# Kernel tuning notes

Hardware: AMD Instinct MI355X
Metric: run time of the kernel (lower is better)

Reference implementation:

```python
import jax, jax.numpy as jnp
import numpy as np

DIM = 12       # model width (l1 out, S5 H)
SEQ = 1600     # SAMPLE_LEN, fixed by BatchNorm1d(SAMPLE_LEN)
P = 8          # STATE_DIM
BATCH = 1024
EPS = 1e-5


def setup_inputs() -> dict:
    key = jax.random.key(0)
    ks = jax.random.split(key, 16)
    rn = lambda k, shape, s=1.0: jax.random.normal(k, shape, jnp.float32) * s
    inp = {}
    inp["x"] = rn(ks[0], (BATCH, SEQ, 1))
    inp["l1_w"] = rn(ks[1], (DIM, 1), 0.5)
    inp["l1_b"] = rn(ks[2], (DIM,), 0.1)
    inp["l2_w"] = rn(ks[3], (1, DIM), 0.3)
    inp["l2_b"] = rn(ks[4], (1,), 0.1)
    inp["bn_gamma"] = jnp.ones((SEQ,), jnp.float32)
    inp["bn_beta"] = jnp.zeros((SEQ,), jnp.float32)
    # S5 parameters for the 3 stacked layers (s5, s5b, s5c), stacked on axis 0.
    # HiPPO-like init: stable (negative real) diagonal, imaginary parts ~ pi*k.
    inp["lam_re"] = -jax.random.uniform(ks[5], (3, P), jnp.float32, 0.1, 1.0)
    inp["lam_im"] = jnp.broadcast_to(np.pi * jnp.arange(P, dtype=jnp.float32), (3, P)) \
                    + 0.1 * rn(ks[6], (3, P))
    inp["b_re"] = rn(ks[7], (3, P, DIM), 1.0 / np.sqrt(DIM))
    inp["b_im"] = rn(ks[8], (3, P, DIM), 1.0 / np.sqrt(DIM))
    inp["c_re"] = rn(ks[9], (3, DIM, P), 1.0 / np.sqrt(P))
    inp["c_im"] = rn(ks[10], (3, DIM, P), 1.0 / np.sqrt(P))
    inp["d"] = rn(ks[11], (3, DIM))
    inp["log_step"] = jnp.log(jax.random.uniform(ks[12], (3, P), jnp.float32, 1e-3, 1e-1))
    return inp


def _s5_layer(u, lam_re, lam_im, b_re, b_im, c_re, c_im, d, log_step):
    """S5 diagonal SSM: ZOH discretization + parallel associative scan.
    u: [B, L, H] real. Returns [B, L, H] real."""
    step = jnp.exp(log_step)                               # [P]
    lam = (lam_re + 1j * lam_im).astype(jnp.complex64)     # [P]
    lam_bar = jnp.exp(lam * step)                          # [P]
    b_bar = ((lam_bar - 1.0) / lam)[:, None] * (b_re + 1j * b_im)  # [P, H]
    # Bu_k = B_bar @ u_k  -> [B, L, P] complex
    bu = (u @ b_bar.real.T) + 1j * (u @ b_bar.imag.T)
    a = jnp.broadcast_to(lam_bar, bu.shape)                # [B, L, P]

    def combine(e1, e2):
        a1, s1 = e1
        a2, s2 = e2
        return a1 * a2, a2 * s1 + s2

    _, xs = jax.lax.associative_scan(combine, (a, bu), axis=1)  # x_k states
    c = c_re + 1j * c_im                                   # [H, P]
    y = 2.0 * jnp.einsum('blp,hp->blh', xs, c).real + u * d
    return y


def reference(x, l1_w, l1_b, l2_w, l2_b, bn_gamma, bn_beta,
              lam_re, lam_im, b_re, b_im, c_re, c_im, d, log_step):
    out = x @ l1_w.T + l1_b                                # [B, L, DIM]
    res = out
    # BatchNorm1d(SEQ) on [B, C=SEQ, L=DIM]: stats over batch and last dim
    mean = out.mean(axis=(0, 2))                           # [SEQ]
    var = out.var(axis=(0, 2))                             # biased, as torch training BN
    out = (out - mean[None, :, None]) * jax.lax.rsqrt(var + EPS)[None, :, None]
    out = out * bn_gamma[None, :, None] + bn_beta[None, :, None]

    out = _s5_layer(out, lam_re[0], lam_im[0], b_re[0], b_im[0], c_re[0], c_im[0], d[0], log_step[0])
    out = jax.nn.relu(out) + res
    res = out
    out = _s5_layer(out, lam_re[1], lam_im[1], b_re[1], b_im[1], c_re[1], c_im[1], d[1], log_step[1])
    out = jax.nn.relu(out) + res
    out = _s5_layer(out, lam_re[2], lam_im[2], b_re[2], b_im[2], c_re[2], c_im[2], d[2], log_step[2])
    return out @ l2_w.T + l2_b                             # [B, L, 1]
```

## Files before the change

kernel.cpp:

```cpp
#include <hip/hip_runtime.h>
#include <cmath>

#define SEQ 1600
#define NB  1024
#define H   12
#define PP  8

typedef float f2 __attribute__((ext_vector_type(2)));

#define O_G0A  0
#define O_G0B  16
#define O_G0C  32
#define O_G1A  48
#define O_G1B  64
#define O_G2A  80
#define O_G2B  96
#define O_LB0R 112
#define O_LB0I 128
#define O_LB1R 144
#define O_LB1I 160
#define O_LB2R 176
#define O_LB2I 192
#define O_C0R  208
#define O_C0I  304
#define O_C1R  400
#define O_C1I  496
#define O_BB1  592
#define O_BB2  784
#define O_FX0  976
#define O_FY0  988
#define O_FZ0  1000
#define O_FW0  1012
#define O_F1X  1024
#define O_F1Y  1036
#define O_F1Z  1048
#define O_CWN  1060
#define O_A6   1076
#define O_A7   1124
#define O_SC   1172
#define PRMF   1174

__device__ __forceinline__ f2 pk_fma_s(f2 a_s, f2 b, f2 c) {
    double d;
    asm("v_pk_fma_f32 %0, %1, %2, %3"
        : "=v"(d)
        : "s"(__builtin_bit_cast(double, a_s)),
          "v"(__builtin_bit_cast(double, b)),
          "v"(__builtin_bit_cast(double, c)));
    return __builtin_bit_cast(f2, d);
}
__device__ __forceinline__ f2 pk_fma_vv(f2 a, f2 b, f2 c) {
    double d;
    asm("v_pk_fma_f32 %0, %1, %2, %3"
        : "=v"(d)
        : "v"(__builtin_bit_cast(double, a)),
          "v"(__builtin_bit_cast(double, b)),
          "v"(__builtin_bit_cast(double, c)));
    return __builtin_bit_cast(f2, d);
}
__device__ __forceinline__ f2 pk_fma_s_blo(f2 a_s, f2 b, f2 c) {
    double d;
    asm("v_pk_fma_f32 %0, %1, %2, %3 op_sel:[0,0,0] op_sel_hi:[1,0,1]"
        : "=v"(d)
        : "s"(__builtin_bit_cast(double, a_s)),
          "v"(__builtin_bit_cast(double, b)),
          "v"(__builtin_bit_cast(double, c)));
    return __builtin_bit_cast(f2, d);
}
__device__ __forceinline__ f2 pk_fma_s_bhi(f2 a_s, f2 b, f2 c) {
    double d;
    asm("v_pk_fma_f32 %0, %1, %2, %3 op_sel:[0,1,0] op_sel_hi:[1,1,1]"
        : "=v"(d)
        : "s"(__builtin_bit_cast(double, a_s)),
          "v"(__builtin_bit_cast(double, b)),
          "v"(__builtin_bit_cast(double, c)));
    return __builtin_bit_cast(f2, d);
}
__device__ __forceinline__ f2 pk_add_s(f2 a_s, f2 b) {
    double d;
    asm("v_pk_add_f32 %0, %1, %2"
        : "=v"(d)
        : "s"(__builtin_bit_cast(double, a_s)),
          "v"(__builtin_bit_cast(double, b)));
    return __builtin_bit_cast(f2, d);
}
__device__ __forceinline__ f2 pk_add_vv(f2 a, f2 b) {
    double d;
    asm("v_pk_add_f32 %0, %1, %2"
        : "=v"(d)
        : "v"(__builtin_bit_cast(double, a)),
          "v"(__builtin_bit_cast(double, b)));
    return __builtin_bit_cast(f2, d);
}
__device__ __forceinline__ f2 cfma_state(f2 s, f2 lbr2_s, f2 lbi2_s, f2 bu) {
    double t, d;
    asm("v_pk_fma_f32 %0, %1, %2, %3 op_sel:[1,0,0] op_sel_hi:[0,1,1] neg_lo:[1,0,0]"
        : "=v"(t)
        : "v"(__builtin_bit_cast(double, s)),
          "s"(__builtin_bit_cast(double, lbi2_s)),
          "v"(__builtin_bit_cast(double, bu)));
    asm("v_pk_fma_f32 %0, %1, %2, %3"
        : "=v"(d)
        : "v"(__builtin_bit_cast(double, s)),
          "s"(__builtin_bit_cast(double, lbr2_s)),
          "v"(t));
    return __builtin_bit_cast(f2, d);
}
__device__ __forceinline__ f2 cmulv(f2 A, f2 B, f2 C) {
    double t, d;
    asm("v_pk_fma_f32 %0, %1, %2, %3 op_sel:[1,1,0] op_sel_hi:[0,1,1] neg_lo:[1,0,0]"
        : "=v"(t)
        : "v"(__builtin_bit_cast(double, B)),
          "v"(__builtin_bit_cast(double, A)),
          "v"(__builtin_bit_cast(double, C)));
    asm("v_pk_fma_f32 %0, %1, %2, %3 op_sel:[0,0,0] op_sel_hi:[1,0,1]"
        : "=v"(d)
        : "v"(__builtin_bit_cast(double, B)),
          "v"(__builtin_bit_cast(double, A)),
          "v"(t));
    return __builtin_bit_cast(f2, d);
}

__global__ __launch_bounds__(256) void k_stats1(const float* __restrict__ x,
                                                float* __restrict__ pS,
                                                float* __restrict__ pQ) {
    int l = blockIdx.x * 256 + threadIdx.x;
    if (l >= SEQ) return;
    int b0 = blockIdx.y * 64;
    float s = 0.f, q = 0.f;
    for (int b = 0; b < 64; ++b) {
        float v = x[(size_t)(b0 + b) * SEQ + l];
        s += v; q += v * v;
    }
    pS[blockIdx.y * SEQ + l] = s;
    pQ[blockIdx.y * SEQ + l] = q;
}

__global__ __launch_bounds__(256)
void k_stats2prep(const float* __restrict__ pS, const float* __restrict__ pQ,
                  const float* __restrict__ w1, const float* __restrict__ b1,
                  const float* __restrict__ gam, const float* __restrict__ bet,
                  float* __restrict__ scale, float* __restrict__ shift,
                  const float* __restrict__ l2w, const float* __restrict__ l2b,
                  const float* __restrict__ lamr, const float* __restrict__ lami,
                  const float* __restrict__ bre, const float* __restrict__ bim,
                  const float* __restrict__ cre, const float* __restrict__ cim,
                  const float* __restrict__ dv,  const float* __restrict__ lstep,
                  float* __restrict__ gprm) {
    const int t = threadIdx.x;
    if (blockIdx.x < 7) {
        int l = blockIdx.x * 256 + t;
        if (l >= SEQ) return;
        float wm = 0, wq = 0, wb = 0, bm = 0, bq = 0;
        for (int h = 0; h < H; h++) {
            float w = w1[h], b = b1[h];
            wm += w; wq += w * w; wb += w * b; bm += b; bq += b * b;
        }
        const float inv = 1.f / 12.f;
        wm *= inv; wq *= inv; wb *= inv; bm *= inv; bq *= inv;
        float s = 0, q = 0;
        for (int k = 0; k < 16; k++) { s += pS[k * SEQ + l]; q += pQ[k * SEQ + l]; }
        float ex = s * (1.f / NB), exx = q * (1.f / NB);
        float mean = ex * wm + bm;
        float e2   = exx * wq + 2.f * ex * wb + bq;
        float var  = e2 - mean * mean;
        float sc   = gam[l] * rsqrtf(var + 1e-5f);
        scale[l] = sc;
        shift[l] = bet[l] - mean * sc;
        return;
    }
    if (t < 48) {
        int h2 = t >> 3, p = t & 7, h = 2 * h2;
        gprm[O_C0R + 2 * t]     = 2.f * cre[h * PP + p];
        gprm[O_C0R + 2 * t + 1] = 2.f * cre[(h + 1) * PP + p];
        gprm[O_C0I + 2 * t]     = -2.f * cim[h * PP + p];
        gprm[O_C0I + 2 * t + 1] = -2.f * cim[(h + 1) * PP + p];
        gprm[O_C1R + 2 * t]     = 2.f * cre[96 + h * PP + p];
        gprm[O_C1R + 2 * t + 1] = 2.f * cre[96 + (h + 1) * PP + p];
        gprm[O_C1I + 2 * t]     = -2.f * cim[96 + h * PP + p];
        gprm[O_C1I + 2 * t + 1] = -2.f * cim[96 + (h + 1) * PP + p];
    }
    if (t < 6) {
        int h = 2 * t;
        gprm[O_FX0 + 2 * t] = w1[h] * dv[h];          gprm[O_FX0 + 2 * t + 1] = w1[h + 1] * dv[h + 1];
        gprm[O_FY0 + 2 * t] = b1[h] * dv[h];          gprm[O_FY0 + 2 * t + 1] = b1[h + 1] * dv[h + 1];
        gprm[O_FZ0 + 2 * t] = dv[h];                  gprm[O_FZ0 + 2 * t + 1] = dv[h + 1];
        gprm[O_FW0 + 2 * t] = w1[h] * dv[H + h];      gprm[O_FW0 + 2 * t + 1] = w1[h + 1] * dv[H + h + 1];
        gprm[O_F1X + 2 * t] = b1[h] * dv[H + h];      gprm[O_F1X + 2 * t + 1] = b1[h + 1] * dv[H + h + 1];
        gprm[O_F1Y + 2 * t] = dv[H + h];              gprm[O_F1Y + 2 * t + 1] = dv[H + h + 1];
        gprm[O_F1Z + 2 * t] = l2w[h] * dv[2 * H + h]; gprm[O_F1Z + 2 * t + 1] = l2w[h + 1] * dv[2 * H + h + 1];
    }
    if (t == 0) {
        float s0 = l2b[0], s1 = 0.f;
        for (int h = 0; h < H; h++) {
            float dw = l2w[h] * dv[2 * H + h];
            s0 += b1[h] * dw; s1 += w1[h] * dw;
        }
        gprm[O_SC + 0] = s0; gprm[O_SC + 1] = s1;
    }
    if (t < 24) {
        int L = t >> 3, p = t & 7;
        float stp = expf(lstep[L * PP + p]);
        float lr = lamr[L * PP + p], li = lami[L * PP + p];
        float er = expf(lr * stp);
        float lbr = er * cosf(li * stp), lbi = er * sinf(li * stp);
        float p2r = lbr * lbr - lbi * lbi, p2i = 2.f * lbr * lbi;
        float p4r = p2r * p2r - p2i * p2i, p4i = 2.f * p2r * p2i;
        float p6r = p4r * p2r - p4i * p2i, p6i = p4r * p2i + p4i * p2r;
        float p7r = p6r * lbr - p6i * lbi, p7i = p6r * lbi + p6i * lbr;
        gprm[O_A6 + 2 * (L * PP + p) + 0] = p6r;
        gprm[O_A6 + 2 * (L * PP + p) + 1] = p6i;
        gprm[O_A7 + 2 * (L * PP + p) + 0] = p7r;
        gprm[O_A7 + 2 * (L * PP + p) + 1] = p7i;
        float den = lr * lr + li * li;
        float fr = ((lbr - 1.f) * lr + lbi * li) / den;
        float fi = (lbi * lr - (lbr - 1.f) * li) / den;
        float sAr = 0, sAi = 0, sBr = 0, sBi = 0, sCr = 0, sCi = 0;
        for (int h = 0; h < H; h++) {
            float brr = bre[L * 96 + p * H + h], bii = bim[L * 96 + p * H + h];
            float vr = fr * brr - fi * bii, vi = fr * bii + fi * brr;
            float w = w1[h], bb = b1[h];
            sAr += w * vr; sAi += w * vi; sBr += bb * vr; sBi += bb * vi; sCr += vr; sCi += vi;
            int fidx = 2 * (h * PP + p);
            if (L == 1)      { gprm[O_BB1 + fidx] = vr; gprm[O_BB1 + fidx + 1] = vi; }
            else if (L == 2) { gprm[O_BB2 + fidx] = vr; gprm[O_BB2 + fidx + 1] = vi; }
        }
        if (L == 0) {
            gprm[O_G0A + 2 * p] = sAr; gprm[O_G0A + 2 * p + 1] = sAi;
            gprm[O_G0B + 2 * p] = sBr; gprm[O_G0B + 2 * p + 1] = sBi;
            gprm[O_G0C + 2 * p] = sCr; gprm[O_G0C + 2 * p + 1] = sCi;
            gprm[O_LB0R + 2 * p] = lbr; gprm[O_LB0R + 2 * p + 1] = lbr;
            gprm[O_LB0I + 2 * p] = lbi; gprm[O_LB0I + 2 * p + 1] = lbi;
        } else if (L == 1) {
            gprm[O_G1A + 2 * p] = sAr; gprm[O_G1A + 2 * p + 1] = sAi;
            gprm[O_G1B + 2 * p] = sBr; gprm[O_G1B + 2 * p + 1] = sBi;
            gprm[O_LB1R + 2 * p] = lbr; gprm[O_LB1R + 2 * p + 1] = lbr;
            gprm[O_LB1I + 2 * p] = lbi; gprm[O_LB1I + 2 * p + 1] = lbi;
        } else {
            gprm[O_G2A + 2 * p] = sAr; gprm[O_G2A + 2 * p + 1] = sAi;
            gprm[O_G2B + 2 * p] = sBr; gprm[O_G2B + 2 * p + 1] = sBi;
            gprm[O_LB2R + 2 * p] = lbr; gprm[O_LB2R + 2 * p + 1] = lbr;
            gprm[O_LB2I + 2 * p] = lbi; gprm[O_LB2I + 2 * p + 1] = lbi;
            float swr = 0, swi = 0;
            for (int hh = 0; hh < H; hh++) {
                float wv = l2w[hh];
                swr += wv * cre[192 + hh * PP + p];
                swi += wv * cim[192 + hh * PP + p];
            }
            gprm[O_CWN + 2 * p + 0] = 2.f * swr; gprm[O_CWN + 2 * p + 1] = -2.f * swi;
        }
    }
}

__device__ __forceinline__ void scan_carry256(f2* S, const float2* a_init,
                                              int lane, int w,
                                              float2 (*aggA)[PP], float2 (*aggS)[PP]) {
    const f2 z2 = {0.f, 0.f};
    f2 A[PP];
#pragma unroll
    for (int p = 0; p < PP; p++) { A[p].x = a_init[p].x; A[p].y = a_init[p].y; }
#pragma unroll
    for (int d = 1; d < 64; d <<= 1) {
#pragma unroll
        for (int p = 0; p < PP; p++) {
            f2 fS, fA;
            fS.x = __shfl_up(S[p].x, (unsigned)d, 64);
            fS.y = __shfl_up(S[p].y, (unsigned)d, 64);
            fA.x = __shfl_up(A[p].x, (unsigned)d, 64);
            fA.y = __shfl_up(A[p].y, (unsigned)d, 64);
            if (lane >= d) {
                S[p] = cmulv(A[p], fS, S[p]);
                A[p] = cmulv(A[p], fA, z2);
            }
        }
    }
    __syncthreads();
    if (lane == 63) {
#pragma unroll
        for (int p = 0; p < PP; p++) {
            aggA[w][p] = make_float2(A[p].x, A[p].y);
            aggS[w][p] = make_float2(S[p].x, S[p].y);
        }
    }
    __syncthreads();
    float eSr[PP], eSi[PP], eAr[PP], eAi[PP];
#pragma unroll
    for (int p = 0; p < PP; p++) {
        float sr = __shfl_up(S[p].x, 1u, 64);
        float si = __shfl_up(S[p].y, 1u, 64);
        float ar = __shfl_up(A[p].x, 1u, 64);
        float ai = __shfl_up(A[p].y, 1u, 64);
        eSr[p] = (lane > 0) ? sr : 0.f;
        eSi[p] = (lane > 0) ? si : 0.f;
        eAr[p] = (lane > 0) ? ar : 1.f;
        eAi[p] = (lane > 0) ? ai : 0.f;
    }
    float Pr[PP], Pi[PP];
#pragma unroll
    for (int p = 0; p < PP; p++) { Pr[p] = 0.f; Pi[p] = 0.f; }
    for (int w2 = 0; w2 < w; w2++) {
#pragma unroll
        for (int p = 0; p < PP; p++) {
            float2 a = aggA[w2][p];
            float2 s = aggS[w2][p];
            float nr = a.x * Pr[p] - a.y * Pi[p] + s.x;
            float ni = a.x * Pi[p] + a.y * Pr[p] + s.y;
            Pr[p] = nr; Pi[p] = ni;
        }
    }
#pragma unroll
    for (int p = 0; p < PP; p++) {
        S[p].x = eAr[p] * Pr[p] - eAi[p] * Pi[p] + eSr[p];
        S[p].y = eAr[p] * Pi[p] + eAi[p] * Pr[p] + eSi[p];
    }
}

__global__ __launch_bounds__(256)
void k_main(const float* __restrict__ x,
            const float* __restrict__ gprm,
            const float* __restrict__ g_scale, const float* __restrict__ g_shift,
            float* __restrict__ out) {
    __shared__ float4 xq[SEQ];
    __shared__ float2 aggA[4][PP], aggS[4][PP];
    const int tid = threadIdx.x, b = blockIdx.x;
    for (int i = tid; i < SEQ; i += 256) {
        float xx = x[(size_t)b * SEQ + i];
        float sc = g_scale[i], sh = g_shift[i];
        xq[i] = make_float4(xx * sc, sc, sh, xx);
    }
    __syncthreads();
    const f2* g0a = (const f2*)(gprm + O_G0A);
    const f2* g0b = (const f2*)(gprm + O_G0B);
    const f2* g0c = (const f2*)(gprm + O_G0C);
    const f2* g1a = (const f2*)(gprm + O_G1A);
    const f2* g1b = (const f2*)(gprm + O_G1B);
    const f2* g2a = (const f2*)(gprm + O_G2A);
    const f2* g2b = (const f2*)(gprm + O_G2B);
    const f2* lb0r = (const f2*)(gprm + O_LB0R);
    const f2* lb0i = (const f2*)(gprm + O_LB0I);
    const f2* lb1r = (const f2*)(gprm + O_LB1R);
    const f2* lb1i = (const f2*)(gprm + O_LB1I);
    const f2* lb2r = (const f2*)(gprm + O_LB2R);
    const f2* lb2i = (const f2*)(gprm + O_LB2I);
    const f2* c0r = (const f2*)(gprm + O_C0R);
    const f2* c0i = (const f2*)(gprm + O_C0I);
    const f2* c1r = (const f2*)(gprm + O_C1R);
    const f2* c1i = (const f2*)(gprm + O_C1I);
    const f2* bb1 = (const f2*)(gprm + O_BB1);
    const f2* bb2 = (const f2*)(gprm + O_BB2);
    const f2* fx0 = (const f2*)(gprm + O_FX0);
    const f2* fy0 = (const f2*)(gprm + O_FY0);
    const f2* fz0 = (const f2*)(gprm + O_FZ0);
    const f2* fw0 = (const f2*)(gprm + O_FW0);
    const f2* f1x = (const f2*)(gprm + O_F1X);
    const f2* f1y = (const f2*)(gprm + O_F1Y);
    const f2* f1z = (const f2*)(gprm + O_F1Z);
    const f2* cwn = (const f2*)(gprm + O_CWN);
    const float Sc0 = gprm[O_SC], Sc1 = gprm[O_SC + 1];
    const int w = tid >> 6, lane = tid & 63;
    const int len = (w == 3) ? 7 : 6;
    const int l0 = (w < 3) ? (w * 384 + lane * 6) : (1152 + lane * 7);
    const float2* aLb = (const float2*)(gprm + ((w == 3) ? O_A7 : O_A6));
    float* orow = out + (size_t)b * SEQ;
    const f2 z2 = {0.f, 0.f};

    f2 s0[PP], car0[PP];

#pragma unroll
    for (int p = 0; p < PP; p++) s0[p] = z2;
#pragma unroll 1
    for (int j = 0; j < len; j++) {
        float4 q = xq[l0 + j];
        float xs = q.x, sc = q.y, sh = q.z;
        f2 xs2 = {xs, xs}, sc2 = {sc, sc}, sh2 = {sh, sh};
#pragma unroll
        for (int p = 0; p < PP; p++) {
            f2 bu = pk_fma_s(g0c[p], sh2, z2);
            bu = pk_fma_s(g0b[p], sc2, bu);
            bu = pk_fma_s(g0a[p], xs2, bu);
            s0[p] = cfma_state(s0[p], lb0r[p], lb0i[p], bu);
        }
    }
    scan_carry256(s0, aLb, lane, w, aggA, aggS);
#pragma unroll
    for (int p = 0; p < PP; p++) car0[p] = s0[p];

    f2 s1[PP];
#pragma unroll
    for (int p = 0; p < PP; p++) s1[p] = z2;
#pragma unroll 1
    for (int j = 0; j < len; j++) {
        float4 q = xq[l0 + j];
        float xs = q.x, sc = q.y, sh = q.z, xx = q.w;
        f2 xs2 = {xs, xs}, sc2 = {sc, sc}, sh2 = {sh, sh}, xx2 = {xx, xx};
#pragma unroll
        for (int p = 0; p < PP; p++) {
            f2 bu = pk_fma_s(g0c[p], sh2, z2);
            bu = pk_fma_s(g0b[p], sc2, bu);
            bu = pk_fma_s(g0a[p], xs2, bu);
            s0[p] = cfma_state(s0[p], lb0r[p], lb0i[p], bu);
        }
        f2 r0p[6], t1[PP];
#pragma unroll
        for (int p = 0; p < PP; p++) t1[p] = z2;
#pragma unroll
        for (int h2 = 0; h2 < 6; h2++) {
            f2 acc = z2;
#pragma unroll
            for (int p = 0; p < PP; p++) {
                acc = pk_fma_s_blo(c0r[h2 * PP + p], s0[p], acc);
                acc = pk_fma_s_bhi(c0i[h2 * PP + p], s0[p], acc);
            }
            acc = pk_fma_s(fx0[h2], xs2, acc);
            acc = pk_fma_s(fy0[h2], sc2, acc);
            acc = pk_fma_s(fz0[h2], sh2, acc);
            acc.x = fmaxf(acc.x, 0.f); acc.y = fmaxf(acc.y, 0.f);
            r0p[h2] = acc;
#pragma unroll
            for (int p = 0; p < PP; p++) {
                t1[p] = pk_fma_s_blo(bb1[(2 * h2) * PP + p], acc, t1[p]);
                t1[p] = pk_fma_s_bhi(bb1[(2 * h2 + 1) * PP + p], acc, t1[p]);
            }
        }
#pragma unroll
        for (int p = 0; p < PP; p++) {
            f2 t = pk_fma_s(g1a[p], xx2, t1[p]);
            t = pk_add_s(g1b[p], t);
            s1[p] = cfma_state(s1[p], lb1r[p], lb1i[p], t);
        }
    }
    scan_carry256(s1, aLb + PP, lane, w, aggA, aggS);

    f2 s2[PP];
#pragma unroll
    for (int p = 0; p < PP; p++) { s0[p] = car0[p]; s2[p] = z2; }
#pragma unroll 1
    for (int j = 0; j < len; j++) {
        int l = l0 + j;
        float4 q = xq[l];
        float xs = q.x, sc = q.y, sh = q.z, xx = q.w;
        f2 xs2 = {xs, xs}, sc2 = {sc, sc}, sh2 = {sh, sh}, xx2 = {xx, xx};
#pragma unroll
        for (int p = 0; p < PP; p++) {
            f2 bu = pk_fma_s(g0c[p], sh2, z2);
            bu = pk_fma_s(g0b[p], sc2, bu);
            bu = pk_fma_s(g0a[p], xs2, bu);
            s0[p] = cfma_state(s0[p], lb0r[p], lb0i[p], bu);
        }
        f2 r0p[6], t1[PP];
#pragma unroll
        for (int p = 0; p < PP; p++) t1[p] = z2;
#pragma unroll
        for (int h2 = 0; h2 < 6; h2++) {
            f2 acc = z2;
#pragma unroll
            for (int p = 0; p < PP; p++) {
                acc = pk_fma_s_blo(c0r[h2 * PP + p], s0[p], acc);
                acc = pk_fma_s_bhi(c0i[h2 * PP + p], s0[p], acc);
            }
            acc = pk_fma_s(fx0[h2], xs2, acc);
            acc = pk_fma_s(fy0[h2], sc2, acc);
            acc = pk_fma_s(fz0[h2], sh2, acc);
            acc.x = fmaxf(acc.x, 0.f); acc.y = fmaxf(acc.y, 0.f);
            r0p[h2] = acc;
#pragma unroll
            for (int p = 0; p < PP; p++) {
                t1[p] = pk_fma_s_blo(bb1[(2 * h2) * PP + p], acc, t1[p]);
                t1[p] = pk_fma_s_bhi(bb1[(2 * h2 + 1) * PP + p], acc, t1[p]);
            }
        }
#pragma unroll
        for (int p = 0; p < PP; p++) {
            f2 t = pk_fma_s(g1a[p], xx2, t1[p]);
            t = pk_add_s(g1b[p], t);
            s1[p] = cfma_state(s1[p], lb1r[p], lb1i[p], t);
        }
        f2 t2[PP], op = z2;
#pragma unroll
        for (int p = 0; p < PP; p++) t2[p] = z2;
#pragma unroll
        for (int h2 = 0; h2 < 6; h2++) {
            f2 acc = z2;
#pragma unroll
            for (int p = 0; p < PP; p++) {
                acc = pk_fma_s_blo(c1r[h2 * PP + p], s1[p], acc);
                acc = pk_fma_s_bhi(c1i[h2 * PP + p], s1[p], acc);
            }
            acc = pk_fma_s(f1y[h2], r0p[h2], acc);
            acc = pk_fma_s(fw0[h2], xx2, acc);
            acc = pk_add_s(f1x[h2], acc);
            acc.x = fmaxf(acc.x, 0.f); acc.y = fmaxf(acc.y, 0.f);
            f2 rsp = pk_add_vv(r0p[h2], acc);
            op = pk_fma_s(f1z[h2], rsp, op);
#pragma unroll
            for (int p = 0; p < PP; p++) {
                t2[p] = pk_fma_s_blo(bb2[(2 * h2) * PP + p], rsp, t2[p]);
                t2[p] = pk_fma_s_bhi(bb2[(2 * h2 + 1) * PP + p], rsp, t2[p]);
            }
        }
#pragma unroll
        for (int p = 0; p < PP; p++) {
            f2 t = pk_fma_s(g2a[p], xx2, t2[p]);
            t = pk_add_s(g2b[p], t);
            s2[p] = cfma_state(s2[p], lb2r[p], lb2i[p], t);
        }
        f2 a2 = z2;
#pragma unroll
        for (int p = 0; p < PP; p++) a2 = pk_fma_s(cwn[p], s2[p], a2);
        orow[l] = Sc0 + xx * Sc1 + op.x + op.y + a2.x + a2.y;
    }
    scan_carry256(s2, aLb + 2 * PP, lane, w, aggA, aggS);

    f2 Tn[PP], m[PP];
#pragma unroll
    for (int p = 0; p < PP; p++) {
        float cwr = gprm[O_CWN + 2 * p], cwi = -gprm[O_CWN + 2 * p + 1];
        float trr = cwr * s2[p].x - cwi * s2[p].y;
        float tii = cwr * s2[p].y + cwi * s2[p].x;
        Tn[p].x = trr; Tn[p].y = -tii;
        m[p].x = gprm[O_LB2R + 2 * p];
        m[p].y = gprm[O_LB2I + 2 * p];
    }
#pragma unroll 1
    for (int j = 0; j < len; j++) {
        f2 cacc = z2;
#pragma unroll
        for (int p = 0; p < PP; p++) cacc = pk_fma_vv(m[p], Tn[p], cacc);
        orow[l0 + j] += cacc.x + cacc.y;
#pragma unroll
        for (int p = 0; p < PP; p++)
            m[p] = cfma_state(m[p], lb2r[p], lb2i[p], z2);
    }
}

extern "C" void kernel_launch(void* const* d_in, const int* in_sizes, int n_in,
                              void* d_out, int out_size, void* d_ws, size_t ws_size,
                              hipStream_t stream) {
    const float* x     = (const float*)d_in[0];
    const float* l1w   = (const float*)d_in[1];
    const float* l1b   = (const float*)d_in[2];
    const float* l2w   = (const float*)d_in[3];
    const float* l2b   = (const float*)d_in[4];
    const float* gam   = (const float*)d_in[5];
    const float* bet   = (const float*)d_in[6];
    const float* lamr  = (const float*)d_in[7];
    const float* lami  = (const float*)d_in[8];
    const float* bre   = (const float*)d_in[9];
    const float* bim   = (const float*)d_in[10];
    const float* cre   = (const float*)d_in[11];
    const float* cim   = (const float*)d_in[12];
    const float* dv    = (const float*)d_in[13];
    const float* lstep = (const float*)d_in[14];
    float* out = (float*)d_out;

    float* wsf     = (float*)d_ws;
    float* w_scale = wsf;
    float* w_shift = wsf + SEQ;
    float* pS      = wsf + 2 * SEQ;
    float* pQ      = pS + 16 * SEQ;
    float* gprm    = pQ + 16 * SEQ;

    k_stats1<<<dim3(7, 16), 256, 0, stream>>>(x, pS, pQ);
    k_stats2prep<<<dim3(8), 256, 0, stream>>>(pS, pQ, l1w, l1b, gam, bet,
                                              w_scale, w_shift,
                                              l2w, l2b, lamr, lami,
                                              bre, bim, cre, cim, dv, lstep, gprm);
    k_main<<<dim3(NB), 256, 0, stream>>>(x, gprm, w_scale, w_shift, out);
}
```

Measured before the change: 197.8 us.

## Split each sequence scan across 512 threads with 3-4 steps per thread

Doubles the block to 512 threads (8 waves), so each thread scans 3 or 4 timesteps instead of 6 or 7. The per-chunk decay powers change from lambda^6/7 to lambda^3/4, and the cross-wave carry now chains 8 wave aggregates. This adds parallelism and shortens the serial per-thread loops. In exchange it adds more scan-carry overhead per step and puts more register pressure on occupancy at 512 threads.

```diff
diff --git a/kernel.cpp b/kernel.cpp
--- a/kernel.cpp
+++ b/kernel.cpp
@@ -5,6 +5,7 @@
 #define NB  1024
 #define H   12
 #define PP  8
+#define NW  8
 
 typedef float f2 __attribute__((ext_vector_type(2)));
 
@@ -35,8 +36,8 @@
 #define O_F1Y  1036
 #define O_F1Z  1048
 #define O_CWN  1060
-#define O_A6   1076
-#define O_A7   1124
+#define O_A3   1076
+#define O_A4   1124
 #define O_SC   1172
 #define PRMF   1174
 
@@ -205,13 +206,12 @@
         float er = expf(lr * stp);
         float lbr = er * cosf(li * stp), lbi = er * sinf(li * stp);
         float p2r = lbr * lbr - lbi * lbi, p2i = 2.f * lbr * lbi;
+        float p3r = p2r * lbr - p2i * lbi, p3i = p2r * lbi + p2i * lbr;
         float p4r = p2r * p2r - p2i * p2i, p4i = 2.f * p2r * p2i;
-        float p6r = p4r * p2r - p4i * p2i, p6i = p4r * p2i + p4i * p2r;
-        float p7r = p6r * lbr - p6i * lbi, p7i = p6r * lbi + p6i * lbr;
-        gprm[O_A6 + 2 * (L * PP + p) + 0] = p6r;
-        gprm[O_A6 + 2 * (L * PP + p) + 1] = p6i;
-        gprm[O_A7 + 2 * (L * PP + p) + 0] = p7r;
-        gprm[O_A7 + 2 * (L * PP + p) + 1] = p7i;
+        gprm[O_A3 + 2 * (L * PP + p) + 0] = p3r;
+        gprm[O_A3 + 2 * (L * PP + p) + 1] = p3i;
+        gprm[O_A4 + 2 * (L * PP + p) + 0] = p4r;
+        gprm[O_A4 + 2 * (L * PP + p) + 1] = p4i;
         float den = lr * lr + li * li;
         float fr = ((lbr - 1.f) * lr + lbi * li) / den;
         float fi = (lbi * lr - (lbr - 1.f) * li) / den;
@@ -252,7 +252,7 @@
     }
 }
 
-__device__ __forceinline__ void scan_carry256(f2* S, const float2* a_init,
+__device__ __forceinline__ void scan_carry512(f2* S, const float2* a_init,
                                               int lane, int w,
                                               float2 (*aggA)[PP], float2 (*aggS)[PP]) {
     const f2 z2 = {0.f, 0.f};
@@ -315,15 +315,15 @@
     }
 }
 
-__global__ __launch_bounds__(256)
+__global__ __launch_bounds__(512)
 void k_main(const float* __restrict__ x,
             const float* __restrict__ gprm,
             const float* __restrict__ g_scale, const float* __restrict__ g_shift,
             float* __restrict__ out) {
     __shared__ float4 xq[SEQ];
-    __shared__ float2 aggA[4][PP], aggS[4][PP];
+    __shared__ float2 aggA[NW][PP], aggS[NW][PP];
     const int tid = threadIdx.x, b = blockIdx.x;
-    for (int i = tid; i < SEQ; i += 256) {
+    for (int i = tid; i < SEQ; i += 512) {
         float xx = x[(size_t)b * SEQ + i];
         float sc = g_scale[i], sh = g_shift[i];
         xq[i] = make_float4(xx * sc, sc, sh, xx);
@@ -358,9 +358,9 @@
     const f2* cwn = (const f2*)(gprm + O_CWN);
     const float Sc0 = gprm[O_SC], Sc1 = gprm[O_SC + 1];
     const int w = tid >> 6, lane = tid & 63;
-    const int len = (w == 3) ? 7 : 6;
-    const int l0 = (w < 3) ? (w * 384 + lane * 6) : (1152 + lane * 7);
-    const float2* aLb = (const float2*)(gprm + ((w == 3) ? O_A7 : O_A6));
+    const int len = (w == 7) ? 4 : 3;
+    const int l0 = (w < 7) ? (tid * 3) : (1344 + lane * 4);
+    const float2* aLb = (const float2*)(gprm + ((w == 7) ? O_A4 : O_A3));
     float* orow = out + (size_t)b * SEQ;
     const f2 z2 = {0.f, 0.f};
 
@@ -381,7 +381,7 @@
             s0[p] = cfma_state(s0[p], lb0r[p], lb0i[p], bu);
         }
     }
-    scan_carry256(s0, aLb, lane, w, aggA, aggS);
+    scan_carry512(s0, aLb, lane, w, aggA, aggS);
 #pragma unroll
     for (int p = 0; p < PP; p++) car0[p] = s0[p];
 
@@ -429,7 +429,7 @@
             s1[p] = cfma_state(s1[p], lb1r[p], lb1i[p], t);
         }
     }
-    scan_carry256(s1, aLb + PP, lane, w, aggA, aggS);
+    scan_carry512(s1, aLb + PP, lane, w, aggA, aggS);
 
     f2 s2[PP];
 #pragma unroll
@@ -509,7 +509,7 @@
         for (int p = 0; p < PP; p++) a2 = pk_fma_s(cwn[p], s2[p], a2);
         orow[l] = Sc0 + xx * Sc1 + op.x + op.y + a2.x + a2.y;
     }
-    scan_carry256(s2, aLb + 2 * PP, lane, w, aggA, aggS);
+    scan_carry512(s2, aLb + 2 * PP, lane, w, aggA, aggS);
 
     f2 Tn[PP], m[PP];
 #pragma unroll
@@ -565,5 +565,5 @@
                                               w_scale, w_shift,
                                               l2w, l2b, lamr, lami,
                                               bre, bim, cre, cim, dv, lstep, gprm);
-    k_main<<<dim3(NB), 256, 0, stream>>>(x, gprm, w_scale, w_shift, out);
-}
+    k_main<<<dim3(NB), 512, 0, stream>>>(x, gprm, w_scale, w_shift, out);
+}
```

New measurement: 296.4 us. +49.8%, slower.
